# Performance work log

Hardware: AMD Instinct MI355X
Metric: run time of the kernel (lower is better)

Reference implementation:

```python
import jax, jax.numpy as jnp
import numpy as np

D_MODEL = 1024
NUM_HEADS = 16
HEAD_DIM = D_MODEL // NUM_HEADS


def setup_inputs() -> dict:
    key = jax.random.key(0)
    ks = jax.random.split(key, 9)
    B, S = 2, 2048
    s = 1.0 / np.sqrt(D_MODEL)
    inp = {
        "x": jax.random.normal(ks[0], (B, S, D_MODEL), dtype=jnp.float32),
        "Wq": jax.random.normal(ks[1], (D_MODEL, D_MODEL), dtype=jnp.float32) * s,
        "bq": jnp.zeros((D_MODEL,), dtype=jnp.float32),
        "Wk": jax.random.normal(ks[2], (D_MODEL, D_MODEL), dtype=jnp.float32) * s,
        "bk": jnp.zeros((D_MODEL,), dtype=jnp.float32),
        "Wv": jax.random.normal(ks[3], (D_MODEL, D_MODEL), dtype=jnp.float32) * s,
        "bv": jnp.zeros((D_MODEL,), dtype=jnp.float32),
        "Wo": jax.random.normal(ks[4], (D_MODEL, D_MODEL), dtype=jnp.float32) * s,
        "bo": jnpp if False else jnp.zeros((D_MODEL,), dtype=jnp.float32),
    }
    return inp


def reference(x, Wq, bq, Wk, bk, Wv, bv, Wo, bo):
    B, S, D = x.shape
    H, hd = NUM_HEADS, HEAD_DIM
    # QKV projections (Linear: x @ W^T + b), split into heads -> [B,H,S,hd]
    q = (x @ Wq.T + bq).reshape(B, S, H, hd).transpose(0, 2, 1, 3)
    k = (x @ Wk.T + bk).reshape(B, S, H, hd).transpose(0, 2, 1, 3)
    v = (x @ Wv.T + bv).reshape(B, S, H, hd).transpose(0, 2, 1, 3)
    # scores [B,H,S,S]
    scores = jnp.einsum('bhqd,bhkd->bhqk', q, k) / jnp.sqrt(jnp.float32(hd))
    p = jax.nn.softmax(scores, axis=-1)
    out = jnp.einsum('bhqk,bhkd->bhqd', p, v)  # [B,H,S,hd]
    out = out.transpose(0, 2, 1, 3).reshape(B, S, D)
    return out @ Wo.T + bo
```

## Files before the change

kernel.cpp:

```cpp
#include <hip/hip_runtime.h>
#include <hip/hip_bf16.h>
#include <math.h>

typedef __bf16 bf16;
typedef unsigned short u16;
typedef __bf16 bf16x8 __attribute__((ext_vector_type(8)));
typedef float  f32x4  __attribute__((ext_vector_type(4)));

#define D_MODEL 1024
#define NHEAD   16
#define HD      64
#define BATCH   2
#define SEQ     2048
#define MTOT    (BATCH*SEQ)

#define EXPSCALE 0.18033688011116016f

__device__ __forceinline__ void async16(const void* g, void* l) {
    __builtin_amdgcn_global_load_lds(
        (__attribute__((address_space(1))) unsigned int*)g,
        (__attribute__((address_space(3))) unsigned int*)l,
        16, 0, 0);
}

__global__ __launch_bounds__(256) void cast_kernel(
    const float* __restrict__ x,
    const float* __restrict__ wq, const float* __restrict__ wk,
    const float* __restrict__ wv, const float* __restrict__ wo,
    bf16* __restrict__ xb, bf16* __restrict__ wqb, bf16* __restrict__ wkb,
    bf16* __restrict__ wvb, bf16* __restrict__ wob)
{
    const int z = blockIdx.y;
    const float* src;
    bf16* dst;
    int n;
    if (z == 0)      { src = x;  dst = xb;  n = MTOT * D_MODEL; }
    else if (z == 1) { src = wq; dst = wqb; n = D_MODEL * D_MODEL; }
    else if (z == 2) { src = wk; dst = wkb; n = D_MODEL * D_MODEL; }
    else if (z == 3) { src = wv; dst = wvb; n = D_MODEL * D_MODEL; }
    else             { src = wo; dst = wob; n = D_MODEL * D_MODEL; }

    int i = (blockIdx.x * 256 + threadIdx.x) * 8;
    if (i >= n) return;
    float4 a = *(const float4*)(src + i);
    float4 b = *(const float4*)(src + i + 4);
    bf16x8 o;
    o[0] = (bf16)a.x; o[1] = (bf16)a.y; o[2] = (bf16)a.z; o[3] = (bf16)a.w;
    o[4] = (bf16)b.x; o[5] = (bf16)b.y; o[6] = (bf16)b.z; o[7] = (bf16)b.w;
    *(bf16x8*)(dst + i) = o;
}

__device__ __forceinline__ void gemm_core(const bf16* __restrict__ A,
                                          const bf16* __restrict__ W,
                                          int m0, int n0,
                                          f32x4 acc[4][4],
                                          u16* lA, u16* lB)
{
    const int tid  = threadIdx.x;
    const int lane = tid & 63;
    const int wave = tid >> 6;
    const int wr   = wave >> 1;
    const int wc   = wave & 1;
    const int fr   = lane & 15;
    const int quad = lane >> 4;

    #pragma unroll
    for (int mi = 0; mi < 4; ++mi)
        #pragma unroll
        for (int ni = 0; ni < 4; ++ni)
            #pragma unroll
            for (int e = 0; e < 4; ++e)
                acc[mi][ni][e] = 0.0f;

    const int row = tid >> 3;
    const int ca  = ((tid & 7) ^ (row & 7)) * 8;
    const bf16* gA[4];
    const bf16* gB[4];
    u16 *sA[4], *sB[4];
    #pragma unroll
    for (int c = 0; c < 4; ++c) {
        int slot = tid + c * 256;
        int r    = row + c * 32;
        gA[c] = A + (size_t)(m0 + r) * 1024 + ca;
        gB[c] = W + (size_t)(n0 + r) * 1024 + ca;
        sA[c] = lA + (size_t)slot * 8;
        sB[c] = lB + (size_t)slot * 8;
    }

    for (int kt = 0; kt < 1024 / 64; ++kt) {
        __syncthreads();
        #pragma unroll
        for (int c = 0; c < 4; ++c) {
            async16(gA[c] + kt * 64, sA[c]);
            async16(gB[c] + kt * 64, sB[c]);
        }
        __syncthreads();

        #pragma unroll
        for (int ks = 0; ks < 2; ++ks) {
            const int sa = ((ks * 4 + quad) ^ (fr & 7)) * 8;
            bf16x8 af[4], bfm[4];
            #pragma unroll
            for (int mi = 0; mi < 4; ++mi)
                af[mi] = *(const bf16x8*)(lA + (wr * 64 + mi * 16 + fr) * 64 + sa);
            #pragma unroll
            for (int ni = 0; ni < 4; ++ni)
                bfm[ni] = *(const bf16x8*)(lB + (wc * 64 + ni * 16 + fr) * 64 + sa);

            #pragma unroll
            for (int mi = 0; mi < 4; ++mi)
                #pragma unroll
                for (int ni = 0; ni < 4; ++ni)
                    acc[mi][ni] = __builtin_amdgcn_mfma_f32_16x16x32_bf16(
                        af[mi], bfm[ni], acc[mi][ni], 0, 0, 0);
        }
    }
}

__global__ __launch_bounds__(256) void qkv_kernel(
    const bf16* __restrict__ x,
    const bf16* __restrict__ Wq, const bf16* __restrict__ Wk, const bf16* __restrict__ Wv,
    const float* __restrict__ bq, const float* __restrict__ bk, const float* __restrict__ bv,
    bf16* __restrict__ Q, bf16* __restrict__ K, bf16* __restrict__ Vt)
{
    __shared__ __align__(16) u16 lA[128 * 64];
    __shared__ __align__(16) u16 lB[128 * 64];

    const int z = blockIdx.z;
    int m0, n0;
    const bf16 *mA, *mB;
    const float* bias;
    if (z == 2) {
        mA = Wv; mB = x; bias = bv;
        m0 = blockIdx.y * 128;
        n0 = blockIdx.x * 128;
    } else {
        mA = x;  mB = (z == 0) ? Wq : Wk; bias = (z == 0) ? bq : bk;
        m0 = blockIdx.x * 128;
        n0 = blockIdx.y * 128;
    }

    f32x4 acc[4][4];
    gemm_core(mA, mB, m0, n0, acc, lA, lB);

    const int lane = threadIdx.x & 63;
    const int wave = threadIdx.x >> 6;
    const int wr = wave >> 1, wc = wave & 1;
    const int col = lane & 15, quad = lane >> 4;

    if (z == 2) {
        #pragma unroll
        for (int mi = 0; mi < 4; ++mi) {
            #pragma unroll
            for (int ni = 0; ni < 4; ++ni) {
                #pragma unroll
                for (int r = 0; r < 4; ++r) {
                    int f = m0 + wr * 64 + mi * 16 + quad * 4 + r;
                    int t = n0 + wc * 64 + ni * 16 + col;
                    float v = acc[mi][ni][r] + bias[f];
                    int b = t >> 11, s = t & 2047;
                    int h = f >> 6,  d = f & 63;
                    Vt[((size_t)(b * NHEAD + h) * HD + d) * SEQ + s] = (bf16)v;
                }
            }
        }
    } else {
        const float qs = (z == 0) ? EXPSCALE : 1.0f;
        bf16* o = (z == 0) ? Q : K;
        #pragma unroll
        for (int mi = 0; mi < 4; ++mi) {
            #pragma unroll
            for (int ni = 0; ni < 4; ++ni) {
                #pragma unroll
                for (int r = 0; r < 4; ++r) {
                    int m = m0 + wr * 64 + mi * 16 + quad * 4 + r;
                    int n = n0 + wc * 64 + ni * 16 + col;
                    float v = (acc[mi][ni][r] + bias[n]) * qs;
                    int b = m >> 11, s = m & 2047;
                    int h = n >> 6,  d = n & 63;
                    o[((size_t)(b * NHEAD + h) * SEQ + s) * HD + d] = (bf16)v;
                }
            }
        }
    }
}

__global__ __launch_bounds__(256, 2) void attn_kernel(
    const bf16* __restrict__ Q, const bf16* __restrict__ K,
    const bf16* __restrict__ Vt, bf16* __restrict__ O)
{
    __shared__ __align__(16) u16 lK[2][128 * 64];
    __shared__ __align__(16) u16 lV[2][64 * 128];

    const int tid  = threadIdx.x;
    const int lane = tid & 63;
    const int wave = tid >> 6;
    const int col  = lane & 15;
    const int quad = lane >> 4;
    const int bh   = blockIdx.x;
    const int q0   = blockIdx.y * 128;
    const int NT   = SEQ / 128;

    const bf16* Qh = Q  + (size_t)bh * SEQ * HD;
    const bf16* Kh = K  + (size_t)bh * SEQ * HD;
    const bf16* Vh = Vt + (size_t)bh * HD * SEQ;

    bf16x8 qf[2][2];
    #pragma unroll
    for (int qb = 0; qb < 2; ++qb)
        #pragma unroll
        for (int ks = 0; ks < 2; ++ks)
            qf[qb][ks] = *(const bf16x8*)(
                Qh + (size_t)(q0 + wave * 32 + qb * 16 + col) * HD + ks * 32 + quad * 8);

    f32x4 acc_o[2][4];
    #pragma unroll
    for (int qb = 0; qb < 2; ++qb)
        #pragma unroll
        for (int nd = 0; nd < 4; ++nd)
            #pragma unroll
            for (int e = 0; e < 4; ++e) acc_o[qb][nd][e] = 0.0f;
    float rs[2] = {0.0f, 0.0f};
    const f32x4 zero4 = {0.0f, 0.0f, 0.0f, 0.0f};

    const int r0  = tid >> 3;
    const int jp  = (((r0 >> 2) & 3) << 3) | (((r0 >> 4) & 1) << 2) | (r0 & 3);
    const int gk0 = ((tid & 7) ^ (r0 & 7)) * 8;
    const bf16* gKc[4];
    #pragma unroll
    for (int c = 0; c < 4; ++c)
        gKc[c] = Kh + (size_t)(c * 32 + jp) * HD + gk0;

    const int vr0 = tid >> 4;
    const int gv0 = ((tid & 15) ^ (vr0 & 7)) * 8;
    const bf16* gVc[4];
    #pragma unroll
    for (int c = 0; c < 4; ++c)
        gVc[c] = Vh + (size_t)(vr0 + c * 16) * SEQ + gv0;

    const int so = tid * 8;

    #pragma unroll
    for (int c = 0; c < 4; ++c)
        async16(gKc[c], lK[0] + so + c * 2048);

    bf16x8 pa0[4], pa1[4];

    for (int jt = 0; jt < NT; ++jt) {
        __syncthreads();

        if (jt + 1 < NT) {
            u16* kd = lK[(jt + 1) & 1];
            #pragma unroll
            for (int c = 0; c < 4; ++c)
                async16(gKc[c] + (size_t)(jt + 1) * 128 * HD, kd + so + c * 2048);
        }
        {
            u16* vd = lV[jt & 1];
            #pragma unroll
            for (int c = 0; c < 4; ++c)
                async16(gVc[c] + jt * 128, vd + so + c * 2048);
        }

        const u16* K_ = lK[jt & 1];

        __builtin_amdgcn_s_setprio(1);

        f32x4 sc0[8], sc1[8];
        #pragma unroll
        for (int nj = 0; nj < 8; ++nj) {
            bf16x8 kf0 = *(const bf16x8*)(
                K_ + (nj * 16 + col) * 64 + ((0 + quad) ^ (col & 7)) * 8);
            sc0[nj] = __builtin_amdgcn_mfma_f32_16x16x32_bf16(kf0, qf[0][0], zero4, 0, 0, 0);
            sc1[nj] = __builtin_amdgcn_mfma_f32_16x16x32_bf16(kf0, qf[1][0], zero4, 0, 0, 0);
        }
        #pragma unroll
        for (int nj = 0; nj < 8; ++nj) {
            bf16x8 kf1 = *(const bf16x8*)(
                K_ + (nj * 16 + col) * 64 + ((4 + quad) ^ (col & 7)) * 8);
            sc0[nj] = __builtin_amdgcn_mfma_f32_16x16x32_bf16(kf1, qf[0][1], sc0[nj], 0, 0, 0);
            sc1[nj] = __builtin_amdgcn_mfma_f32_16x16x32_bf16(kf1, qf[1][1], sc1[nj], 0, 0, 0);
        }

        if (jt > 0) {
            const u16* V_ = lV[(jt - 1) & 1];
            #pragma unroll
            for (int c = 0; c < 4; ++c) {
                #pragma unroll
                for (int nd = 0; nd < 4; ++nd) {
                    int row = nd * 16 + col;
                    int jb  = (c * 4 + quad) ^ (row & 7);
                    bf16x8 vb = *(const bf16x8*)(V_ + row * 128 + jb * 8);
                    acc_o[0][nd] = __builtin_amdgcn_mfma_f32_16x16x32_bf16(
                        pa0[c], vb, acc_o[0][nd], 0, 0, 0);
                    acc_o[1][nd] = __builtin_amdgcn_mfma_f32_16x16x32_bf16(
                        pa1[c], vb, acc_o[1][nd], 0, 0, 0);
                }
            }
        }

        __builtin_amdgcn_s_setprio(0);

        #pragma unroll
        for (int c = 0; c < 4; ++c) {
            bf16x8 t0, t1;
            #pragma unroll
            for (int e = 0; e < 4; ++e) {
                float a = __builtin_amdgcn_exp2f(sc0[2 * c][e]);
                float b = __builtin_amdgcn_exp2f(sc0[2 * c + 1][e]);
                rs[0] += a + b;
                t0[e]     = (bf16)a;
                t0[4 + e] = (bf16)b;
                float a1 = __builtin_amdgcn_exp2f(sc1[2 * c][e]);
                float b1 = __builtin_amdgcn_exp2f(sc1[2 * c + 1][e]);
                rs[1] += a1 + b1;
                t1[e]     = (bf16)a1;
                t1[4 + e] = (bf16)b1;
            }
            pa0[c] = t0;
            pa1[c] = t1;
        }
    }

    __syncthreads();

    {
        const u16* V_ = lV[(NT - 1) & 1];
        #pragma unroll
        for (int c = 0; c < 4; ++c) {
            #pragma unroll
            for (int nd = 0; nd < 4; ++nd) {
                int row = nd * 16 + col;
                int jb  = (c * 4 + quad) ^ (row & 7);
                bf16x8 vb = *(const bf16x8*)(V_ + row * 128 + jb * 8);
                acc_o[0][nd] = __builtin_amdgcn_mfma_f32_16x16x32_bf16(
                    pa0[c], vb, acc_o[0][nd], 0, 0, 0);
                acc_o[1][nd] = __builtin_amdgcn_mfma_f32_16x16x32_bf16(
                    pa1[c], vb, acc_o[1][nd], 0, 0, 0);
            }
        }
    }

    const int b = bh >> 4, h = bh & 15;
    #pragma unroll
    for (int qb = 0; qb < 2; ++qb) {
        float v = rs[qb];
        v += __shfl_xor(v, 16);
        v += __shfl_xor(v, 32);
        float inv = 1.0f / v;
        float invr[4];
        #pragma unroll
        for (int r = 0; r < 4; ++r)
            invr[r] = __shfl(inv, quad * 4 + r);
        #pragma unroll
        for (int nd = 0; nd < 4; ++nd) {
            #pragma unroll
            for (int r = 0; r < 4; ++r) {
                int srow = q0 + wave * 32 + qb * 16 + quad * 4 + r;
                int d    = nd * 16 + col;
                float o  = acc_o[qb][nd][r] * invr[r];
                O[((size_t)(b * SEQ + srow)) * D_MODEL + h * HD + d] = (bf16)o;
            }
        }
    }
}

__global__ __launch_bounds__(256) void oproj_kernel(
    const bf16* __restrict__ A, const bf16* __restrict__ Wo,
    const float* __restrict__ bo, float* __restrict__ out)
{
    __shared__ __align__(16) u16 lA[128 * 64];
    __shared__ __align__(16) u16 lB[64 * 64];

    const int m0 = blockIdx.x * 128;
    const int n0 = blockIdx.y * 64;

    const int tid  = threadIdx.x;
    const int lane = tid & 63;
    const int wave = tid >> 6;
    const int wr   = wave >> 1;
    const int wc   = wave & 1;
    const int fr   = lane & 15;
    const int quad = lane >> 4;

    f32x4 acc[4][2];
    #pragma unroll
    for (int mi = 0; mi < 4; ++mi)
        #pragma unroll
        for (int ni = 0; ni < 2; ++ni)
            #pragma unroll
            for (int e = 0; e < 4; ++e)
                acc[mi][ni][e] = 0.0f;

    const int row = tid >> 3;
    const int ca  = ((tid & 7) ^ (row & 7)) * 8;
    const bf16* gA[4];
    u16* sA[4];
    #pragma unroll
    for (int c = 0; c < 4; ++c) {
        int slot = tid + c * 256;
        gA[c] = A + (size_t)(m0 + row + c * 32) * 1024 + ca;
        sA[c] = lA + (size_t)slot * 8;
    }
    const bf16* gB[2];
    u16* sB[2];
    #pragma unroll
    for (int c = 0; c < 2; ++c) {
        int slot = tid + c * 256;
        gB[c] = Wo + (size_t)(n0 + row + c * 32) * 1024 + ca;
        sB[c] = lB + (size_t)slot * 8;
    }

    for (int kt = 0; kt < 1024 / 64; ++kt) {
        __syncthreads();
        #pragma unroll
        for (int c = 0; c < 4; ++c) async16(gA[c] + kt * 64, sA[c]);
        #pragma unroll
        for (int c = 0; c < 2; ++c) async16(gB[c] + kt * 64, sB[c]);
        __syncthreads();

        #pragma unroll
        for (int ks = 0; ks < 2; ++ks) {
            const int sa = ((ks * 4 + quad) ^ (fr & 7)) * 8;
            bf16x8 af[4], bfm[2];
            #pragma unroll
            for (int mi = 0; mi < 4; ++mi)
                af[mi] = *(const bf16x8*)(lA + (wr * 64 + mi * 16 + fr) * 64 + sa);
            #pragma unroll
            for (int ni = 0; ni < 2; ++ni)
                bfm[ni] = *(const bf16x8*)(lB + (wc * 32 + ni * 16 + fr) * 64 + sa);

            #pragma unroll
            for (int mi = 0; mi < 4; ++mi)
                #pragma unroll
                for (int ni = 0; ni < 2; ++ni)
                    acc[mi][ni] = __builtin_amdgcn_mfma_f32_16x16x32_bf16(
                        af[mi], bfm[ni], acc[mi][ni], 0, 0, 0);
        }
    }

    const int col = fr;
    #pragma unroll
    for (int mi = 0; mi < 4; ++mi) {
        #pragma unroll
        for (int ni = 0; ni < 2; ++ni) {
            #pragma unroll
            for (int r = 0; r < 4; ++r) {
                int m = m0 + wr * 64 + mi * 16 + quad * 4 + r;
                int n = n0 + wc * 32 + ni * 16 + col;
                out[(size_t)m * D_MODEL + n] = acc[mi][ni][r] + bo[n];
            }
        }
    }
}

extern "C" void kernel_launch(void* const* d_in, const int* in_sizes, int n_in,
                              void* d_out, int out_size, void* d_ws, size_t ws_size,
                              hipStream_t stream)
{
    const float* x  = (const float*)d_in[0];
    const float* Wq = (const float*)d_in[1];
    const float* bq = (const float*)d_in[2];
    const float* Wk = (const float*)d_in[3];
    const float* bk = (const float*)d_in[4];
    const float* Wv = (const float*)d_in[5];
    const float* bv = (const float*)d_in[6];
    const float* Wo = (const float*)d_in[7];
    const float* bo = (const float*)d_in[8];
    float* out = (float*)d_out;

    char* ws = (char*)d_ws;
    const size_t XSZ = (size_t)MTOT * D_MODEL * sizeof(bf16);
    const size_t WSZ = (size_t)D_MODEL * D_MODEL * sizeof(bf16);
    bf16* wqb = (bf16*)(ws);
    bf16* wkb = (bf16*)(ws + WSZ);
    bf16* wvb = (bf16*)(ws + 2 * WSZ);
    bf16* wob = (bf16*)(ws + 3 * WSZ);
    bf16* xb  = (bf16*)(ws + 4 * WSZ);
    bf16* Qb  = (bf16*)(ws + 4 * WSZ + XSZ);
    bf16* Kb  = (bf16*)(ws + 4 * WSZ + 2 * XSZ);
    bf16* Vt  = (bf16*)(ws + 4 * WSZ + 3 * XSZ);
    bf16* At  = (bf16*)(ws + 4 * WSZ + 4 * XSZ);

    cast_kernel<<<dim3((MTOT * D_MODEL) / (256 * 8), 5), 256, 0, stream>>>(
        x, Wq, Wk, Wv, Wo, xb, wqb, wkb, wvb, wob);

    qkv_kernel<<<dim3(32, 8, 3), 256, 0, stream>>>(
        xb, wqb, wkb, wvb, bq, bk, bv, Qb, Kb, Vt);

    attn_kernel<<<dim3(BATCH * NHEAD, SEQ / 128), 256, 0, stream>>>(Qb, Kb, Vt, At);

    oproj_kernel<<<dim3(MTOT / 128, D_MODEL / 64), 256, 0, stream>>>(At, wob, bo, out);
}
```

Measured before the change: 183.3 us.

## Double-buffer LDS tiles in QKV and output-projection GEMMs

Both projection GEMMs now keep two LDS stages: the first K-tile is loaded before the loop, and each iteration issues the async global-to-LDS loads for the next tile before running MFMAs on the current one. This drops one barrier per iteration and lets global load latency overlap with matrix math. In exchange LDS use per block doubles (64 KB for QKV, 48 KB for the output projection), which may reduce how many blocks fit on each compute unit.

```diff
diff --git a/kernel.cpp b/kernel.cpp
--- a/kernel.cpp
+++ b/kernel.cpp
@@ -87,14 +87,26 @@
         sB[c] = lB + (size_t)slot * 8;
     }
 
+    #pragma unroll
+    for (int c = 0; c < 4; ++c) {
+        async16(gA[c], sA[c]);
+        async16(gB[c], sB[c]);
+    }
+
     for (int kt = 0; kt < 1024 / 64; ++kt) {
         __syncthreads();
-        #pragma unroll
-        for (int c = 0; c < 4; ++c) {
-            async16(gA[c] + kt * 64, sA[c]);
-            async16(gB[c] + kt * 64, sB[c]);
-        }
-        __syncthreads();
+
+        const int cur = (kt & 1) * 8192;
+        if (kt + 1 < 1024 / 64) {
+            const int nx = ((kt + 1) & 1) * 8192;
+            #pragma unroll
+            for (int c = 0; c < 4; ++c) {
+                async16(gA[c] + (kt + 1) * 64, sA[c] + nx);
+                async16(gB[c] + (kt + 1) * 64, sB[c] + nx);
+            }
+        }
+        const u16* bA = lA + cur;
+        const u16* bB = lB + cur;
 
         #pragma unroll
         for (int ks = 0; ks < 2; ++ks) {
@@ -102,10 +114,10 @@
             bf16x8 af[4], bfm[4];
             #pragma unroll
             for (int mi = 0; mi < 4; ++mi)
-                af[mi] = *(const bf16x8*)(lA + (wr * 64 + mi * 16 + fr) * 64 + sa);
+                af[mi] = *(const bf16x8*)(bA + (wr * 64 + mi * 16 + fr) * 64 + sa);
             #pragma unroll
             for (int ni = 0; ni < 4; ++ni)
-                bfm[ni] = *(const bf16x8*)(lB + (wc * 64 + ni * 16 + fr) * 64 + sa);
+                bfm[ni] = *(const bf16x8*)(bB + (wc * 64 + ni * 16 + fr) * 64 + sa);
 
             #pragma unroll
             for (int mi = 0; mi < 4; ++mi)
@@ -123,8 +135,8 @@
     const float* __restrict__ bq, const float* __restrict__ bk, const float* __restrict__ bv,
     bf16* __restrict__ Q, bf16* __restrict__ K, bf16* __restrict__ Vt)
 {
-    __shared__ __align__(16) u16 lA[128 * 64];
-    __shared__ __align__(16) u16 lB[128 * 64];
+    __shared__ __align__(16) u16 lA[2 * 128 * 64];
+    __shared__ __align__(16) u16 lB[2 * 128 * 64];
 
     const int z = blockIdx.z;
     int m0, n0;
@@ -369,8 +381,8 @@
     const bf16* __restrict__ A, const bf16* __restrict__ Wo,
     const float* __restrict__ bo, float* __restrict__ out)
 {
-    __shared__ __align__(16) u16 lA[128 * 64];
-    __shared__ __align__(16) u16 lB[64 * 64];
+    __shared__ __align__(16) u16 lA[2 * 128 * 64];
+    __shared__ __align__(16) u16 lB[2 * 64 * 64];
 
     const int m0 = blockIdx.x * 128;
     const int n0 = blockIdx.y * 64;
@@ -411,13 +423,26 @@
         sB[c] = lB + (size_t)slot * 8;
     }
 
+    #pragma unroll
+    for (int c = 0; c < 4; ++c) async16(gA[c], sA[c]);
+    #pragma unroll
+    for (int c = 0; c < 2; ++c) async16(gB[c], sB[c]);
+
     for (int kt = 0; kt < 1024 / 64; ++kt) {
         __syncthreads();
-        #pragma unroll
-        for (int c = 0; c < 4; ++c) async16(gA[c] + kt * 64, sA[c]);
-        #pragma unroll
-        for (int c = 0; c < 2; ++c) async16(gB[c] + kt * 64, sB[c]);
-        __syncthreads();
+
+        const int curA = (kt & 1) * 8192;
+        const int curB = (kt & 1) * 4096;
+        if (kt + 1 < 1024 / 64) {
+            const int nxA = ((kt + 1) & 1) * 8192;
+            const int nxB = ((kt + 1) & 1) * 4096;
+            #pragma unroll
+            for (int c = 0; c < 4; ++c) async16(gA[c] + (kt + 1) * 64, sA[c] + nxA);
+            #pragma unroll
+            for (int c = 0; c < 2; ++c) async16(gB[c] + (kt + 1) * 64, sB[c] + nxB);
+        }
+        const u16* bA = lA + curA;
+        const u16* bB = lB + curB;
 
         #pragma unroll
         for (int ks = 0; ks < 2; ++ks) {
@@ -425,10 +450,10 @@
             bf16x8 af[4], bfm[2];
             #pragma unroll
             for (int mi = 0; mi < 4; ++mi)
-                af[mi] = *(const bf16x8*)(lA + (wr * 64 + mi * 16 + fr) * 64 + sa);
+                af[mi] = *(const bf16x8*)(bA + (wr * 64 + mi * 16 + fr) * 64 + sa);
             #pragma unroll
             for (int ni = 0; ni < 2; ++ni)
-                bfm[ni] = *(const bf16x8*)(lB + (wc * 32 + ni * 16 + fr) * 64 + sa);
+                bfm[ni] = *(const bf16x8*)(bB + (wc * 32 + ni * 16 + fr) * 64 + sa);
 
             #pragma unroll
             for (int mi = 0; mi < 4; ++mi)
```

Measured after the change: 185.3 us. Within noise of the previous version (+1.1%).
